# Kernel optimization log

Hardware: AMD Instinct MI355X
Metric: run time of the kernel (lower is better)

The kernel has to match this reference:

```python
import jax, jax.numpy as jnp
import numpy as np

B, A, N, D = 512, 3, 64, 32


def _lte(x):
    """LTETransform: straight-through hard threshold (forward: 1[x>0], backward: identity)."""
    hard = (x > 0).astype(x.dtype)
    return x + jax.lax.stop_gradient(hard - x)


def setup_inputs() -> dict:
    key = jax.random.key(0)
    k1, k2 = jax.random.split(key)
    feature = jax.random.normal(k1, (B, N, D), dtype=jnp.float32)
    indicator = jax.random.normal(k2, (A, N, D), dtype=jnp.float32)
    return {"feature": feature, "indicator": indicator}


def reference(feature, indicator):
    # gate = LTE(DotWeight(indicator[0], indicator[1])) -> [N, N]
    gate = _lte(jnp.einsum('id,jd->ij', indicator[0], indicator[1]))

    # QKV[a,i,j,:,:] = indicator[a,i,:] (outer) indicator[a,j,:]  (rank-1), so
    # input[b,a,i,j,d] = (feature[b,i,:] . indicator[a,i,:]) * indicator[a,j,d]
    s = jnp.einsum('bnd,and->ban', feature, indicator)  # [B, 3, N]

    # query[b,i,j,d] = elu(s[b,0,i] * ind[0,j,d]) + 1              [B,N,N,D]
    q = jax.nn.elu(s[:, 0, :, None, None] * indicator[0][None, None, :, :]) + 1.0
    # key.transpose(1,2)[b,i,j,d] = elu(s[b,1,j] * ind[1,i,d]) + 1  [B,N,N,D]
    k_t = jax.nn.elu(s[:, 1, None, :, None] * indicator[1][None, :, None, :]) + 1.0

    score = jnp.einsum('bijd,bijd->bij', q, k_t)  # [B, N, N]
    probs = jax.nn.softmax(score, axis=-1)
    score_hat = probs * gate[None, :, :]

    # value[b,i,j,d] = s[b,2,i] * ind[2,j,d];  out = sum_j scoreHat * value
    out = s[:, 2, :, None] * jnp.einsum('bij,jd->bid', score_hat, indicator[2])
    return out  # [B, N, D]
```

## Files before the change

### kernel.cpp

```cpp
#include <hip/hip_runtime.h>

namespace {
constexpr int N   = 64;
constexpr int D   = 32;
constexpr int PD  = 36;
constexpr int SHP = 72;
constexpr float LOG2E = 1.4426950408889634f;
constexpr float LN2   = 0.6931471805599453f;

typedef float f32x2 __attribute__((ext_vector_type(2)));

#if __has_builtin(__builtin_amdgcn_exp2f)
__device__ __forceinline__ float fexp2(float x) { return __builtin_amdgcn_exp2f(x); }
#else
__device__ __forceinline__ float fexp2(float x) { return exp2f(x); }
#endif
#if __has_builtin(__builtin_amdgcn_rcpf)
__device__ __forceinline__ float frcp(float x) { return __builtin_amdgcn_rcpf(x); }
#else
__device__ __forceinline__ float frcp(float x) { return 1.0f / x; }
#endif
__device__ __forceinline__ void wavebar() {
#if __has_builtin(__builtin_amdgcn_wave_barrier)
    __builtin_amdgcn_wave_barrier();
#endif
}

__global__ __launch_bounds__(512, 4) void fused(
        const float* __restrict__ feature,
        const float* __restrict__ ind,
        float* __restrict__ out) {
    __shared__ float ind_lds[3][N][PD];
    __shared__ float s_lds[3][N];
    __shared__ float sh_lds[N][SHP];

    const int t    = threadIdx.x;
    const int lane = t & 63;
    const int wave = t >> 6;
    const int b    = blockIdx.x;

    {
        const float4* src = reinterpret_cast<const float4*>(ind);
#pragma unroll
        for (int idx = t; idx < 3 * N * D / 4; idx += 512) {
            int a = idx >> 9;
            int r = idx & 511;
            int n = r >> 3;
            int k = r & 7;
            *reinterpret_cast<float4*>(&ind_lds[a][n][k * 4]) = src[idx];
        }
    }

    if (t < 3 * N) {
        int a = t >> 6, n = t & 63;
        const float4* frow = reinterpret_cast<const float4*>(feature + ((size_t)b * N + n) * D);
        const float4* irow = reinterpret_cast<const float4*>(ind + (a * N + n) * D);
        f32x2 sa2 = {0.f, 0.f};
#pragma unroll
        for (int k = 0; k < 8; ++k) {
            float4 f4 = frow[k];
            float4 i4 = irow[k];
            sa2 = __builtin_elementwise_fma(f32x2{f4.x, f4.y}, f32x2{i4.x, i4.y}, sa2);
            sa2 = __builtin_elementwise_fma(f32x2{f4.z, f4.w}, f32x2{i4.z, i4.w}, sa2);
        }
        s_lds[a][n] = sa2.x + sa2.y;
    }
    __syncthreads();

    int igu[8];
#pragma unroll
    for (int r = 0; r < 8; ++r)
        igu[r] = __builtin_amdgcn_readfirstlane(wave * 8 + r);

    unsigned long long gmask[8];
    {
        f32x2 wv[16];
#pragma unroll
        for (int k4 = 0; k4 < 8; ++k4) {
            float4 w4 = *reinterpret_cast<const float4*>(&ind_lds[1][lane][k4 * 4]);
            wv[k4 * 2 + 0] = f32x2{w4.x, w4.y};
            wv[k4 * 2 + 1] = f32x2{w4.z, w4.w};
        }
#pragma unroll
        for (int r = 0; r < 8; ++r) {
            f32x2 ga = {0.f, 0.f};
#pragma unroll
            for (int k4 = 0; k4 < 8; ++k4) {
                float4 a4 = *reinterpret_cast<const float4*>(ind + igu[r] * D + k4 * 4);
                ga = __builtin_elementwise_fma(f32x2{a4.x, a4.y}, wv[k4 * 2 + 0], ga);
                ga = __builtin_elementwise_fma(f32x2{a4.z, a4.w}, wv[k4 * 2 + 1], ga);
            }
            gmask[r] = __ballot(ga.x + ga.y > 0.f);
        }
    }

    const float s1Ls = s_lds[1][lane] * LOG2E;
    const f32x2 s1L  = {s1Ls, s1Ls};
    const f32x2 ln2v = {LN2, LN2};
    const f32x2 onev = {1.0f, 1.0f};
    const f32x2 zerv = {0.0f, 0.0f};

    float s0v[8];
#pragma unroll
    for (int r = 0; r < 8; ++r) s0v[r] = s_lds[0][wave * 8 + r] * LOG2E;

    f32x2 sc2[8] = {{0.f, 0.f}, {0.f, 0.f}, {0.f, 0.f}, {0.f, 0.f},
                    {0.f, 0.f}, {0.f, 0.f}, {0.f, 0.f}, {0.f, 0.f}};

#define SCORE_BODY(NEGA, FMAA, AM, FM)                                              \
    {                                                                               \
        const f32x2 amv = {(AM), (AM)};                                             \
        const f32x2 fmv = {(FM), (FM)};                                             \
        f32x2 acc = sc2[r];                                                         \
        _Pragma("unroll")                                                           \
        for (int k4 = 0; k4 < 4; ++k4) {                                            \
            float4 v4 = *reinterpret_cast<const float4*>(                           \
                ind + N * D + igu[r] * D + c * 16 + k4 * 4);            \
            f32x2 vp[2] = {f32x2{v4.x, v4.y}, f32x2{v4.z, v4.w}};                   \
            _Pragma("unroll")                                                       \
            for (int h = 0; h < 2; ++h) {                                           \
                f32x2 aneg = amv * NEGA[k4 * 2 + h];                                \
                f32x2 A    = __builtin_elementwise_fma(fmv, FMAA[k4 * 2 + h], onev);\
                f32x2 bL   = s1L * vp[h];                                           \
                f32x2 bneg = __builtin_elementwise_min(bL, zerv);                   \
                f32x2 B    = __builtin_elementwise_fma(                             \
                    __builtin_elementwise_max(bL, zerv), ln2v, onev);               \
                f32x2 mn   = aneg + bneg;                                           \
                f32x2 E    = {fexp2(mn.x), fexp2(mn.y)};                            \
                acc = __builtin_elementwise_fma(E * A, B, acc);                     \
            }                                                                       \
        }                                                                           \
        sc2[r] = acc;                                                               \
    }

#pragma unroll
    for (int c = 0; c < 2; ++c) {
        f32x2 un[8], upl[8];
#pragma unroll
        for (int k4 = 0; k4 < 4; ++k4) {
            float4 v = *reinterpret_cast<const float4*>(&ind_lds[0][lane][c * 16 + k4 * 4]);
            f32x2 x0 = {v.x, v.y}, x1 = {v.z, v.w};
            f32x2 n0 = __builtin_elementwise_min(x0, zerv);
            f32x2 n1 = __builtin_elementwise_min(x1, zerv);
            un[k4 * 2 + 0]  = n0;
            un[k4 * 2 + 1]  = n1;
            upl[k4 * 2 + 0] = (x0 - n0) * ln2v;
            upl[k4 * 2 + 1] = (x1 - n1) * ln2v;
        }
#pragma unroll
        for (int r = 0; r < 8; ++r) {
            const float s0u = __uint_as_float(
                __builtin_amdgcn_readfirstlane(__float_as_uint(s0v[r])));
            if (s0u >= 0.f) {
                SCORE_BODY(un, upl, s0u, s0u)
            } else {
                SCORE_BODY(upl, un, s0u * LOG2E, s0u * LN2)
            }
        }
    }
#undef SCORE_BODY

    float score[8];
#pragma unroll
    for (int r = 0; r < 8; ++r) score[r] = sc2[r].x + sc2[r].y;

    float mx[8], e[8], sm[8];
#pragma unroll
    for (int r = 0; r < 8; ++r) mx[r] = score[r];
#pragma unroll
    for (int off = 32; off >= 1; off >>= 1) {
#pragma unroll
        for (int r = 0; r < 8; ++r) mx[r] = fmaxf(mx[r], __shfl_xor(mx[r], off));
    }
#pragma unroll
    for (int r = 0; r < 8; ++r) e[r] = fexp2((score[r] - mx[r]) * LOG2E);
#pragma unroll
    for (int r = 0; r < 8; ++r) sm[r] = e[r];
#pragma unroll
    for (int off = 32; off >= 1; off >>= 1) {
#pragma unroll
        for (int r = 0; r < 8; ++r) sm[r] += __shfl_xor(sm[r], off);
    }
#pragma unroll
    for (int r = 0; r < 8; ++r) {
        const int ig  = wave * 8 + r;
        const float g = (float)((gmask[r] >> lane) & 1ull);
        sh_lds[ig][lane] = (e[r] * g) * (s_lds[2][ig] * frcp(sm[r]));
    }

    wavebar();

    {
        const int i_loc = t >> 3;
        const int dq    = t & 7;
        f32x2 acc0 = {0.f, 0.f}, acc1 = {0.f, 0.f};
#pragma unroll
        for (int j = 0; j < 64; j += 4) {
            float4 sh4 = *reinterpret_cast<const float4*>(&sh_lds[i_loc][j]);
#pragma unroll
            for (int c = 0; c < 4; ++c) {
                float4 v4 = *reinterpret_cast<const float4*>(&ind_lds[2][j + c][dq * 4]);
                float  w  = (&sh4.x)[c];
                f32x2 wvv = {w, w};
                acc0 = __builtin_elementwise_fma(wvv, f32x2{v4.x, v4.y}, acc0);
                acc1 = __builtin_elementwise_fma(wvv, f32x2{v4.z, v4.w}, acc1);
            }
        }
        float4 acc = {acc0.x, acc0.y, acc1.x, acc1.y};
        *reinterpret_cast<float4*>(out + ((size_t)b * N + i_loc) * D + dq * 4) = acc;
    }
}
}

extern "C" void kernel_launch(void* const* d_in, const int* in_sizes, int n_in,
                              void* d_out, int out_size, void* d_ws, size_t ws_size,
                              hipStream_t stream) {
    const float* feature = (const float*)d_in[0];
    const float* ind     = (const float*)d_in[1];
    float*       out     = (float*)d_out;
    fused<<<512, 512, 0, stream>>>(feature, ind, out);
}
```

Before: 79.53 us.

## Compute score transposed with hoisted key splits, staging through shared memory

The score computation is reorganised so each lane owns a column index i and each wave iterates over j rows. The min/max split of the key indicator row is precomputed once in registers, and the uniform s1 value selects the sign branch. Query indicator rows are read from global memory with a double-buffered prefetch. Because the lane mapping no longer matches the softmax layout, scores are written to a padded shared-memory tile and read back transposed after a block barrier. This adds LDS traffic and a __syncthreads in exchange for fewer per-element ops in the exp-heavy inner loop.

```diff
diff --git a/kernel.cpp b/kernel.cpp
--- a/kernel.cpp
+++ b/kernel.cpp
@@ -5,6 +5,7 @@
 constexpr int D   = 32;
 constexpr int PD  = 36;
 constexpr int SHP = 72;
+constexpr int SCP = 65;
 constexpr float LOG2E = 1.4426950408889634f;
 constexpr float LN2   = 0.6931471805599453f;
 
@@ -32,6 +33,7 @@
         float* __restrict__ out) {
     __shared__ float ind_lds[3][N][PD];
     __shared__ float s_lds[3][N];
+    __shared__ float sc_lds[N][SCP];
     __shared__ float sh_lds[N][SHP];
 
     const int t    = threadIdx.x;
@@ -72,7 +74,12 @@
     for (int r = 0; r < 8; ++r)
         igu[r] = __builtin_amdgcn_readfirstlane(wave * 8 + r);
 
+    const f32x2 ln2v = {LN2, LN2};
+    const f32x2 onev = {1.0f, 1.0f};
+    const f32x2 zerv = {0.0f, 0.0f};
+
     unsigned long long gmask[8];
+    f32x2 u1n[16], u1p[16];
     {
         f32x2 wv[16];
 #pragma unroll
@@ -92,77 +99,72 @@
             }
             gmask[r] = __ballot(ga.x + ga.y > 0.f);
         }
-    }
-
-    const float s1Ls = s_lds[1][lane] * LOG2E;
-    const f32x2 s1L  = {s1Ls, s1Ls};
-    const f32x2 ln2v = {LN2, LN2};
-    const f32x2 onev = {1.0f, 1.0f};
-    const f32x2 zerv = {0.0f, 0.0f};
-
-    float s0v[8];
-#pragma unroll
-    for (int r = 0; r < 8; ++r) s0v[r] = s_lds[0][wave * 8 + r] * LOG2E;
-
-    f32x2 sc2[8] = {{0.f, 0.f}, {0.f, 0.f}, {0.f, 0.f}, {0.f, 0.f},
-                    {0.f, 0.f}, {0.f, 0.f}, {0.f, 0.f}, {0.f, 0.f}};
-
-#define SCORE_BODY(NEGA, FMAA, AM, FM)                                              \
-    {                                                                               \
-        const f32x2 amv = {(AM), (AM)};                                             \
-        const f32x2 fmv = {(FM), (FM)};                                             \
-        f32x2 acc = sc2[r];                                                         \
-        _Pragma("unroll")                                                           \
-        for (int k4 = 0; k4 < 4; ++k4) {                                            \
-            float4 v4 = *reinterpret_cast<const float4*>(                           \
-                ind + N * D + igu[r] * D + c * 16 + k4 * 4);            \
-            f32x2 vp[2] = {f32x2{v4.x, v4.y}, f32x2{v4.z, v4.w}};                   \
-            _Pragma("unroll")                                                       \
-            for (int h = 0; h < 2; ++h) {                                           \
-                f32x2 aneg = amv * NEGA[k4 * 2 + h];                                \
-                f32x2 A    = __builtin_elementwise_fma(fmv, FMAA[k4 * 2 + h], onev);\
-                f32x2 bL   = s1L * vp[h];                                           \
-                f32x2 bneg = __builtin_elementwise_min(bL, zerv);                   \
-                f32x2 B    = __builtin_elementwise_fma(                             \
-                    __builtin_elementwise_max(bL, zerv), ln2v, onev);               \
-                f32x2 mn   = aneg + bneg;                                           \
-                f32x2 E    = {fexp2(mn.x), fexp2(mn.y)};                            \
-                acc = __builtin_elementwise_fma(E * A, B, acc);                     \
-            }                                                                       \
-        }                                                                           \
-        sc2[r] = acc;                                                               \
-    }
-
-#pragma unroll
-    for (int c = 0; c < 2; ++c) {
-        f32x2 un[8], upl[8];
-#pragma unroll
-        for (int k4 = 0; k4 < 4; ++k4) {
-            float4 v = *reinterpret_cast<const float4*>(&ind_lds[0][lane][c * 16 + k4 * 4]);
-            f32x2 x0 = {v.x, v.y}, x1 = {v.z, v.w};
-            f32x2 n0 = __builtin_elementwise_min(x0, zerv);
-            f32x2 n1 = __builtin_elementwise_min(x1, zerv);
-            un[k4 * 2 + 0]  = n0;
-            un[k4 * 2 + 1]  = n1;
-            upl[k4 * 2 + 0] = (x0 - n0) * ln2v;
-            upl[k4 * 2 + 1] = (x1 - n1) * ln2v;
-        }
-#pragma unroll
-        for (int r = 0; r < 8; ++r) {
-            const float s0u = __uint_as_float(
-                __builtin_amdgcn_readfirstlane(__float_as_uint(s0v[r])));
-            if (s0u >= 0.f) {
-                SCORE_BODY(un, upl, s0u, s0u)
-            } else {
-                SCORE_BODY(upl, un, s0u * LOG2E, s0u * LN2)
+#pragma unroll
+        for (int k = 0; k < 16; ++k) {
+            f32x2 nn = __builtin_elementwise_min(wv[k], zerv);
+            u1n[k] = nn;
+            u1p[k] = wv[k] - nn;
+        }
+    }
+
+    {
+        const float s0Ls = s_lds[0][lane] * LOG2E;
+        const f32x2 s0L2 = {s0Ls, s0Ls};
+
+        float4 buf[2][8];
+#pragma unroll
+        for (int k = 0; k < 8; ++k)
+            buf[0][k] = *reinterpret_cast<const float4*>(ind + igu[0] * D + k * 4);
+
+#pragma unroll
+        for (int jj = 0; jj < 8; ++jj) {
+            if (jj < 7) {
+#pragma unroll
+                for (int k = 0; k < 8; ++k)
+                    buf[(jj + 1) & 1][k] =
+                        *reinterpret_cast<const float4*>(ind + igu[jj + 1] * D + k * 4);
             }
-        }
-    }
-#undef SCORE_BODY
+            const int jgl = wave * 8 + jj;
+            const float s1raw = s_lds[1][jgl];
+            const float s1u = __uint_as_float(
+                __builtin_amdgcn_readfirstlane(__float_as_uint(s1raw)));
+            const float s1e = s1u * LOG2E;
+            const f32x2 s1v  = {s1u, s1u};
+            const f32x2 s1ev = {s1e, s1e};
+            f32x2 acc = {0.f, 0.f};
+
+#define SBODY(UN, UP)                                                           \
+    {                                                                           \
+        _Pragma("unroll")                                                       \
+        for (int k4 = 0; k4 < 8; ++k4) {                                        \
+            const float4 c4 = buf[jj & 1][k4];                                  \
+            const f32x2 u0a = {c4.x, c4.y};                                     \
+            const f32x2 u0b = {c4.z, c4.w};                                     \
+            _Pragma("unroll")                                                   \
+            for (int h = 0; h < 2; ++h) {                                       \
+                const f32x2 u0 = h ? u0b : u0a;                                 \
+                f32x2 aL = s0L2 * u0;                                           \
+                f32x2 an = __builtin_elementwise_min(aL, zerv);                 \
+                f32x2 Af = __builtin_elementwise_fma(aL - an, ln2v, onev);      \
+                f32x2 bn = s1ev * UN[k4 * 2 + h];                               \
+                f32x2 Bf = __builtin_elementwise_fma(s1v, UP[k4 * 2 + h], onev);\
+                f32x2 mn = an + bn;                                             \
+                f32x2 E  = {fexp2(mn.x), fexp2(mn.y)};                          \
+                acc = __builtin_elementwise_fma(E, Af * Bf, acc);               \
+            }                                                                   \
+        }                                                                       \
+    }
+            if (s1u >= 0.f) { SBODY(u1n, u1p) } else { SBODY(u1p, u1n) }
+#undef SBODY
+
+            sc_lds[jgl][lane] = acc.x + acc.y;
+        }
+    }
+    __syncthreads();
 
     float score[8];
 #pragma unroll
-    for (int r = 0; r < 8; ++r) score[r] = sc2[r].x + sc2[r].y;
+    for (int r = 0; r < 8; ++r) score[r] = sc_lds[lane][wave * 8 + r];
 
     float mx[8], e[8], sm[8];
 #pragma unroll
```

Measured after the change: 85.14 us. 1.07x slower.

## Process two batches per 1024-thread block, sharing gate and indicator work

Applied to the files above, without the earlier changes.

Each block now handles two batch elements with 1024 threads, and each wave covers 4 query rows for both batches. This halves the per-batch cost of the gate ballot, the indicator LDS staging and the value-row loads, since the loaded indicator[1] row is reused across both batches. The launch drops to 256 blocks, so fewer blocks may leave some CUs underused, and the 1024-thread blocks may raise register pressure. The sh_lds row pitch also changes from 72 to 68.

```diff
diff --git a/kernel.cpp b/kernel.cpp
--- a/kernel.cpp
+++ b/kernel.cpp
@@ -4,7 +4,7 @@
 constexpr int N   = 64;
 constexpr int D   = 32;
 constexpr int PD  = 36;
-constexpr int SHP = 72;
+constexpr int SHP = 68;
 constexpr float LOG2E = 1.4426950408889634f;
 constexpr float LN2   = 0.6931471805599453f;
 
@@ -26,23 +26,23 @@
 #endif
 }
 
-__global__ __launch_bounds__(512, 4) void fused(
+__global__ __launch_bounds__(1024, 4) void fused(
         const float* __restrict__ feature,
         const float* __restrict__ ind,
         float* __restrict__ out) {
     __shared__ float ind_lds[3][N][PD];
-    __shared__ float s_lds[3][N];
-    __shared__ float sh_lds[N][SHP];
+    __shared__ float s_lds[3][2][N];
+    __shared__ float sh_lds[2][N][SHP];
 
     const int t    = threadIdx.x;
     const int lane = t & 63;
     const int wave = t >> 6;
-    const int b    = blockIdx.x;
+    const int b0   = blockIdx.x << 1;
 
     {
         const float4* src = reinterpret_cast<const float4*>(ind);
 #pragma unroll
-        for (int idx = t; idx < 3 * N * D / 4; idx += 512) {
+        for (int idx = t; idx < 3 * N * D / 4; idx += 1024) {
             int a = idx >> 9;
             int r = idx & 511;
             int n = r >> 3;
@@ -51,9 +51,13 @@
         }
     }
 
-    if (t < 3 * N) {
-        int a = t >> 6, n = t & 63;
-        const float4* frow = reinterpret_cast<const float4*>(feature + ((size_t)b * N + n) * D);
+    if (t < 384) {
+        int a    = t >> 7;
+        int rem  = t & 127;
+        int bsel = rem >> 6;
+        int n    = rem & 63;
+        const float4* frow = reinterpret_cast<const float4*>(
+            feature + ((size_t)(b0 + bsel) * N + n) * D);
         const float4* irow = reinterpret_cast<const float4*>(ind + (a * N + n) * D);
         f32x2 sa2 = {0.f, 0.f};
 #pragma unroll
@@ -63,16 +67,16 @@
             sa2 = __builtin_elementwise_fma(f32x2{f4.x, f4.y}, f32x2{i4.x, i4.y}, sa2);
             sa2 = __builtin_elementwise_fma(f32x2{f4.z, f4.w}, f32x2{i4.z, i4.w}, sa2);
         }
-        s_lds[a][n] = sa2.x + sa2.y;
+        s_lds[a][bsel][n] = sa2.x + sa2.y;
     }
     __syncthreads();
 
-    int igu[8];
-#pragma unroll
-    for (int r = 0; r < 8; ++r)
-        igu[r] = __builtin_amdgcn_readfirstlane(wave * 8 + r);
-
-    unsigned long long gmask[8];
+    int igu[4];
+#pragma unroll
+    for (int r = 0; r < 4; ++r)
+        igu[r] = __builtin_amdgcn_readfirstlane(wave * 4 + r);
+
+    unsigned long long gmask[4];
     {
         f32x2 wv[16];
 #pragma unroll
@@ -82,7 +86,7 @@
             wv[k4 * 2 + 1] = f32x2{w4.z, w4.w};
         }
 #pragma unroll
-        for (int r = 0; r < 8; ++r) {
+        for (int r = 0; r < 4; ++r) {
             f32x2 ga = {0.f, 0.f};
 #pragma unroll
             for (int k4 = 0; k4 < 8; ++k4) {
@@ -94,34 +98,39 @@
         }
     }
 
-    const float s1Ls = s_lds[1][lane] * LOG2E;
-    const f32x2 s1L  = {s1Ls, s1Ls};
+    const float s1L0s = s_lds[1][0][lane] * LOG2E;
+    const float s1L1s = s_lds[1][1][lane] * LOG2E;
+    const f32x2 s1L0 = {s1L0s, s1L0s};
+    const f32x2 s1L1 = {s1L1s, s1L1s};
     const f32x2 ln2v = {LN2, LN2};
     const f32x2 onev = {1.0f, 1.0f};
     const f32x2 zerv = {0.0f, 0.0f};
 
-    float s0v[8];
-#pragma unroll
-    for (int r = 0; r < 8; ++r) s0v[r] = s_lds[0][wave * 8 + r] * LOG2E;
-
-    f32x2 sc2[8] = {{0.f, 0.f}, {0.f, 0.f}, {0.f, 0.f}, {0.f, 0.f},
-                    {0.f, 0.f}, {0.f, 0.f}, {0.f, 0.f}, {0.f, 0.f}};
-
-#define SCORE_BODY(NEGA, FMAA, AM, FM)                                              \
+    float s0v0[4], s0v1[4];
+#pragma unroll
+    for (int r = 0; r < 4; ++r) {
+        s0v0[r] = s_lds[0][0][wave * 4 + r] * LOG2E;
+        s0v1[r] = s_lds[0][1][wave * 4 + r] * LOG2E;
+    }
+
+    f32x2 sc0[4] = {{0.f, 0.f}, {0.f, 0.f}, {0.f, 0.f}, {0.f, 0.f}};
+    f32x2 sc1[4] = {{0.f, 0.f}, {0.f, 0.f}, {0.f, 0.f}, {0.f, 0.f}};
+
+#define SBODY(ACC, NEGA, FMAA, AM, FM, S1V)                                         \
     {                                                                               \
         const f32x2 amv = {(AM), (AM)};                                             \
         const f32x2 fmv = {(FM), (FM)};                                             \
-        f32x2 acc = sc2[r];                                                         \
+        f32x2 acc = ACC;                                                            \
         _Pragma("unroll")                                                           \
         for (int k4 = 0; k4 < 4; ++k4) {                                            \
-            float4 v4 = *reinterpret_cast<const float4*>(                           \
-                ind + N * D + igu[r] * D + c * 16 + k4 * 4);            \
-            f32x2 vp[2] = {f32x2{v4.x, v4.y}, f32x2{v4.z, v4.w}};                   \
+            const f32x2 vp0 = {vq[k4].x, vq[k4].y};                                 \
+            const f32x2 vp1 = {vq[k4].z, vq[k4].w};                                 \
             _Pragma("unroll")                                                       \
             for (int h = 0; h < 2; ++h) {                                           \
+                const f32x2 vp = h ? vp1 : vp0;                                     \
                 f32x2 aneg = amv * NEGA[k4 * 2 + h];                                \
                 f32x2 A    = __builtin_elementwise_fma(fmv, FMAA[k4 * 2 + h], onev);\
-                f32x2 bL   = s1L * vp[h];                                           \
+                f32x2 bL   = (S1V) * vp;                                            \
                 f32x2 bneg = __builtin_elementwise_min(bL, zerv);                   \
                 f32x2 B    = __builtin_elementwise_fma(                             \
                     __builtin_elementwise_max(bL, zerv), ln2v, onev);               \
@@ -130,7 +139,7 @@
                 acc = __builtin_elementwise_fma(E * A, B, acc);                     \
             }                                                                       \
         }                                                                           \
-        sc2[r] = acc;                                                               \
+        ACC = acc;                                                                  \
     }
 
 #pragma unroll
@@ -148,55 +157,75 @@
             upl[k4 * 2 + 1] = (x1 - n1) * ln2v;
         }
 #pragma unroll
-        for (int r = 0; r < 8; ++r) {
-            const float s0u = __uint_as_float(
-                __builtin_amdgcn_readfirstlane(__float_as_uint(s0v[r])));
-            if (s0u >= 0.f) {
-                SCORE_BODY(un, upl, s0u, s0u)
+        for (int r = 0; r < 4; ++r) {
+            float4 vq[4];
+#pragma unroll
+            for (int k4 = 0; k4 < 4; ++k4)
+                vq[k4] = *reinterpret_cast<const float4*>(
+                    ind + N * D + igu[r] * D + c * 16 + k4 * 4);
+
+            const float s0ua = __uint_as_float(
+                __builtin_amdgcn_readfirstlane(__float_as_uint(s0v0[r])));
+            if (s0ua >= 0.f) {
+                SBODY(sc0[r], un, upl, s0ua, s0ua, s1L0)
             } else {
-                SCORE_BODY(upl, un, s0u * LOG2E, s0u * LN2)
-            }
-        }
-    }
-#undef SCORE_BODY
+                SBODY(sc0[r], upl, un, s0ua * LOG2E, s0ua * LN2, s1L0)
+            }
+            const float s0ub = __uint_as_float(
+                __builtin_amdgcn_readfirstlane(__float_as_uint(s0v1[r])));
+            if (s0ub >= 0.f) {
+                SBODY(sc1[r], un, upl, s0ub, s0ub, s1L1)
+            } else {
+                SBODY(sc1[r], upl, un, s0ub * LOG2E, s0ub * LN2, s1L1)
+            }
+        }
+    }
+#undef SBODY
 
     float score[8];
 #pragma unroll
-    for (int r = 0; r < 8; ++r) score[r] = sc2[r].x + sc2[r].y;
-
+    for (int r = 0; r < 4; ++r) {
+        score[r]     = sc0[r].x + sc0[r].y;
+        score[4 + r] = sc1[r].x + sc1[r].y;
+    }
     float mx[8], e[8], sm[8];
 #pragma unroll
-    for (int r = 0; r < 8; ++r) mx[r] = score[r];
+    for (int q = 0; q < 8; ++q) mx[q] = score[q];
 #pragma unroll
     for (int off = 32; off >= 1; off >>= 1) {
 #pragma unroll
-        for (int r = 0; r < 8; ++r) mx[r] = fmaxf(mx[r], __shfl_xor(mx[r], off));
-    }
-#pragma unroll
-    for (int r = 0; r < 8; ++r) e[r] = fexp2((score[r] - mx[r]) * LOG2E);
-#pragma unroll
-    for (int r = 0; r < 8; ++r) sm[r] = e[r];
+        for (int q = 0; q < 8; ++q) mx[q] = fmaxf(mx[q], __shfl_xor(mx[q], off));
+    }
+#pragma unroll
+    for (int q = 0; q < 8; ++q) e[q] = fexp2((score[q] - mx[q]) * LOG2E);
+#pragma unroll
+    for (int q = 0; q < 8; ++q) sm[q] = e[q];
 #pragma unroll
     for (int off = 32; off >= 1; off >>= 1) {
 #pragma unroll
-        for (int r = 0; r < 8; ++r) sm[r] += __shfl_xor(sm[r], off);
-    }
-#pragma unroll
-    for (int r = 0; r < 8; ++r) {
-        const int ig  = wave * 8 + r;
-        const float g = (float)((gmask[r] >> lane) & 1ull);
-        sh_lds[ig][lane] = (e[r] * g) * (s_lds[2][ig] * frcp(sm[r]));
+        for (int q = 0; q < 8; ++q) sm[q] += __shfl_xor(sm[q], off);
+    }
+#pragma unroll
+    for (int q = 0; q < 8; ++q) {
+        const int bsel = q >> 2;
+        const int rr   = q & 3;
+        const int row  = wave * 4 + rr;
+        const float g  = (float)((gmask[rr] >> lane) & 1ull);
+        sh_lds[bsel][row][lane] =
+            (e[q] * g) * (s_lds[2][bsel][row] * frcp(sm[q]));
     }
 
     wavebar();
 
     {
-        const int i_loc = t >> 3;
-        const int dq    = t & 7;
+        const int ri   = lane >> 3;
+        const int dq   = lane & 7;
+        const int bsel = ri >> 2;
+        const int row  = wave * 4 + (ri & 3);
         f32x2 acc0 = {0.f, 0.f}, acc1 = {0.f, 0.f};
 #pragma unroll
         for (int j = 0; j < 64; j += 4) {
-            float4 sh4 = *reinterpret_cast<const float4*>(&sh_lds[i_loc][j]);
+            float4 sh4 = *reinterpret_cast<const float4*>(&sh_lds[bsel][row][j]);
 #pragma unroll
             for (int c = 0; c < 4; ++c) {
                 float4 v4 = *reinterpret_cast<const float4*>(&ind_lds[2][j + c][dq * 4]);
@@ -207,7 +236,8 @@
             }
         }
         float4 acc = {acc0.x, acc0.y, acc1.x, acc1.y};
-        *reinterpret_cast<float4*>(out + ((size_t)b * N + i_loc) * D + dq * 4) = acc;
+        *reinterpret_cast<float4*>(
+            out + ((size_t)(b0 + bsel) * N + row) * D + dq * 4) = acc;
     }
 }
 }
@@ -218,5 +248,5 @@
     const float* feature = (const float*)d_in[0];
     const float* ind     = (const float*)d_in[1];
     float*       out     = (float*)d_out;
-    fused<<<512, 512, 0, stream>>>(feature, ind, out);
-}
+    fused<<<256, 1024, 0, stream>>>(feature, ind, out);
+}
```

Result: no change. 80.13 us (+0.8%).
